# Optimization experiments

Measured on AMD Instinct MI355X. Metric: run time of the kernel, lower is better.

The kernel has to match this reference:

```python
import jax, jax.numpy as jnp
import numpy as np

HEADS = 8
EMBED = 512


def setup_inputs() -> dict:
    key = jax.random.key(0)
    ks = jax.random.split(key, 9)
    N, KL, QL, S = 4, 512, 32, 64
    D = EMBED // HEADS
    return {
        "values": jax.random.normal(ks[0], (N, KL, EMBED), jnp.float32),
        "keys": jax.random.normal(ks[1], (N, KL, EMBED), jnp.float32),
        "query": jax.random.normal(ks[2], (N, QL, S, EMBED), jnp.float32),
        "mask": jax.random.randint(ks[3], (N, 1, 1, KL, 1), 0, 2, jnp.int32),
        "Wv": jax.random.normal(ks[4], (D, D), jnp.float32) * 0.05,
        "Wk": jax.random.normal(ks[5], (D, D), jnp.float32) * 0.05,
        "Wq": jax.random.normal(ks[6], (D, D), jnp.float32) * 0.05,
        "Wo": jax.random.normal(ks[7], (EMBED, EMBED), jnp.float32) * 0.05,
        "bo": jax.random.normal(ks[8], (EMBED,), jnp.float32) * 0.05,
    }


def reference(values, keys, query, mask, Wv, Wk, Wq, Wo, bo):
    N, KL, E = keys.shape
    QL, S = query.shape[1], query.shape[2]
    H = HEADS
    D = E // H
    # split heads, then per-head linear (weights shared across heads, torch y = x @ W.T)
    v = jnp.einsum('nkhd,ed->nkhe', values.reshape(N, KL, H, D), Wv)
    k = jnp.einsum('nkhd,ed->nkhe', keys.reshape(N, KL, H, D), Wk)
    q = jnp.einsum('nqshd,ed->nqshe', query.reshape(N, QL, S, H, D), Wq)
    # energy: [N, H, QL, KL, S]
    energy = jnp.einsum('nqshd,nkhd->nhqks', q, k)
    energy = jnp.where(mask == 0, jnp.float32(-1e20), energy)
    scale = jnp.float32(E ** 0.5)
    attention = jax.nn.softmax(energy / scale, axis=3)  # softmax over key axis
    out = jnp.einsum('nhqks,nkhd->nqshd', attention, v).reshape(N, QL, S, E)
    return out @ Wo.T + bo
```

## Files before the change

kernel.cpp:

```cpp
#include <hip/hip_runtime.h>
#include <math.h>


typedef __bf16 bf16;
typedef __attribute__((ext_vector_type(8))) __bf16 bf16x8;
typedef __attribute__((ext_vector_type(4))) __bf16 bf16x4;
typedef __attribute__((ext_vector_type(4))) float f32x4;

#define LW 68
#define LS 72
#define QSCALE (0.044194173824159216f * 1.4426950408889634f)
#define MASK_BIAS -64.0f

__device__ __forceinline__ bf16x8 cvt8(const float* p, float s) {
    float4 x0 = *(const float4*)p;
    float4 x1 = *(const float4*)(p + 4);
    bf16x8 r = {(bf16)(x0.x * s), (bf16)(x0.y * s), (bf16)(x0.z * s), (bf16)(x0.w * s),
                (bf16)(x1.x * s), (bf16)(x1.y * s), (bf16)(x1.z * s), (bf16)(x1.w * s)};
    return r;
}

__global__ __launch_bounds__(256, 2) void kv_proj(const float* __restrict__ keys,
                                                  const float* __restrict__ values,
                                                  const float* __restrict__ Wk,
                                                  const float* __restrict__ Wv,
                                                  bf16* __restrict__ Kp,
                                                  bf16* __restrict__ Vt) {
    __shared__ bf16 Xk[64 * LW];
    __shared__ bf16 Xv[64 * LW];
    int t = threadIdx.x;
    int nh = blockIdx.x >> 3, kt = blockIdx.x & 7;
    int n = nh >> 3, h = nh & 7, kl0 = kt * 64;
    int w = t >> 6, quad = (t >> 4) & 3, c16 = t & 15;
#pragma unroll
    for (int i = 0; i < 4; ++i) {
        int f = t + i * 256, row = f >> 4, c4 = f & 15;
        float4 a = *(const float4*)(keys + ((long)n * 512 + kl0 + row) * 512 + h * 64 + c4 * 4);
        float4 b = *(const float4*)(values + ((long)n * 512 + kl0 + row) * 512 + h * 64 + c4 * 4);
        *(bf16x4*)&Xk[row * LW + c4 * 4] = (bf16x4){(bf16)a.x, (bf16)a.y, (bf16)a.z, (bf16)a.w};
        *(bf16x4*)&Xv[row * LW + c4 * 4] = (bf16x4){(bf16)b.x, (bf16)b.y, (bf16)b.z, (bf16)b.w};
    }
    __syncthreads();
    if (w < 2) {
        bf16x8 wf[8];
#pragma unroll
        for (int nb = 0; nb < 4; ++nb)
#pragma unroll
            for (int kc = 0; kc < 2; ++kc)
                wf[nb * 2 + kc] = cvt8(Wk + (16 * nb + c16) * 64 + 32 * kc + quad * 8, 1.0f);
        f32x4 acc[2][4];
#pragma unroll
        for (int mb = 0; mb < 2; ++mb)
#pragma unroll
            for (int nb = 0; nb < 4; ++nb) acc[mb][nb] = (f32x4){0.f, 0.f, 0.f, 0.f};
#pragma unroll
        for (int kc = 0; kc < 2; ++kc) {
            bf16x8 a0 = *(const bf16x8*)&Xk[(32 * w + c16) * LW + 32 * kc + quad * 8];
            bf16x8 a1 = *(const bf16x8*)&Xk[(32 * w + 16 + c16) * LW + 32 * kc + quad * 8];
#pragma unroll
            for (int nb = 0; nb < 4; ++nb) {
                acc[0][nb] = __builtin_amdgcn_mfma_f32_16x16x32_bf16(a0, wf[nb * 2 + kc], acc[0][nb], 0, 0, 0);
                acc[1][nb] = __builtin_amdgcn_mfma_f32_16x16x32_bf16(a1, wf[nb * 2 + kc], acc[1][nb], 0, 0, 0);
            }
        }
#pragma unroll
        for (int mb = 0; mb < 2; ++mb)
#pragma unroll
            for (int nb = 0; nb < 4; ++nb)
#pragma unroll
                for (int r = 0; r < 4; ++r)
                    Kp[((long)nh * 512 + kl0 + 32 * w + 16 * mb + quad * 4 + r) * 64 + 16 * nb + c16] =
                        (bf16)acc[mb][nb][r];
    } else {
        int w2 = w - 2;
        bf16x8 af[4];
#pragma unroll
        for (int mb = 0; mb < 2; ++mb)
#pragma unroll
            for (int kc = 0; kc < 2; ++kc)
                af[mb * 2 + kc] = cvt8(Wv + (32 * w2 + 16 * mb + c16) * 64 + 32 * kc + quad * 8, 1.0f);
        f32x4 acc[2][4];
#pragma unroll
        for (int mb = 0; mb < 2; ++mb)
#pragma unroll
            for (int nb = 0; nb < 4; ++nb) acc[mb][nb] = (f32x4){0.f, 0.f, 0.f, 0.f};
#pragma unroll
        for (int kc = 0; kc < 2; ++kc) {
#pragma unroll
            for (int nb = 0; nb < 4; ++nb) {
                bf16x8 b = *(const bf16x8*)&Xv[(16 * nb + c16) * LW + 32 * kc + quad * 8];
                acc[0][nb] = __builtin_amdgcn_mfma_f32_16x16x32_bf16(af[kc], b, acc[0][nb], 0, 0, 0);
                acc[1][nb] = __builtin_amdgcn_mfma_f32_16x16x32_bf16(af[2 + kc], b, acc[1][nb], 0, 0, 0);
            }
        }
#pragma unroll
        for (int mb = 0; mb < 2; ++mb)
#pragma unroll
            for (int nb = 0; nb < 4; ++nb)
#pragma unroll
                for (int r = 0; r < 4; ++r)
                    Vt[((long)nh * 64 + 32 * w2 + 16 * mb + quad * 4 + r) * 512 + kl0 + 16 * nb + c16] =
                        (bf16)acc[mb][nb][r];
    }
}

__global__ __launch_bounds__(256, 3) void attn(const float* __restrict__ query,
                                               const float* __restrict__ Wq,
                                               const bf16* __restrict__ Kp,
                                               const bf16* __restrict__ Vtg,
                                               const int* __restrict__ mask,
                                               bf16* __restrict__ AO) {
    __shared__ bf16 SX[128 * LS];
    __shared__ bf16 Qt[128 * LW];
    __shared__ bf16 Kt[64 * LW];
    __shared__ bf16 Vs[64 * LW];
    __shared__ float Mb[64];
    int t = threadIdx.x;
    int nh = blockIdx.x & 31, qtile = blockIdx.x >> 5;
    int n = nh >> 3, h = nh & 7;
    int r0 = qtile * 128;
    int w = t >> 6, quad = (t >> 4) & 3, c16 = t & 15;
    const bf16* Kb = Kp + (long)nh * 512 * 64;
    const bf16* Vb = Vtg + (long)nh * 64 * 512;

    int prow0 = t >> 3, pcol0 = t & 7;
    int prow1 = (t + 256) >> 3, pcol1 = t & 7;
    bf16x8 pk0 = *(const bf16x8*)(Kb + (long)prow0 * 64 + pcol0 * 8);
    bf16x8 pk1 = *(const bf16x8*)(Kb + (long)prow1 * 64 + pcol1 * 8);
    bf16x8 pv0 = *(const bf16x8*)(Vb + (long)prow0 * 512 + pcol0 * 8);
    bf16x8 pv1 = *(const bf16x8*)(Vb + (long)prow1 * 512 + pcol1 * 8);
    float mnext = 0.f;
    if (t < 64) mnext = mask[n * 512 + t] ? 0.f : MASK_BIAS;

    bf16x8 wf[8];
#pragma unroll
    for (int nb = 0; nb < 4; ++nb)
#pragma unroll
        for (int kc = 0; kc < 2; ++kc)
            wf[nb * 2 + kc] = cvt8(Wq + (16 * nb + c16) * 64 + 32 * kc + quad * 8, QSCALE);

#pragma unroll
    for (int i = 0; i < 8; ++i) {
        int f = t + i * 256, row = f >> 4, c4 = f & 15;
        float4 a = *(const float4*)(query + ((long)n * 2048 + r0 + row) * 512 + h * 64 + c4 * 4);
        *(bf16x4*)&SX[row * LS + c4 * 4] = (bf16x4){(bf16)a.x, (bf16)a.y, (bf16)a.z, (bf16)a.w};
    }
    __syncthreads();
    {
        f32x4 qa[2][4];
#pragma unroll
        for (int mb = 0; mb < 2; ++mb)
#pragma unroll
            for (int nb = 0; nb < 4; ++nb) qa[mb][nb] = (f32x4){0.f, 0.f, 0.f, 0.f};
#pragma unroll
        for (int kc = 0; kc < 2; ++kc) {
            bf16x8 a0 = *(const bf16x8*)&SX[(32 * w + c16) * LS + 32 * kc + quad * 8];
            bf16x8 a1 = *(const bf16x8*)&SX[(32 * w + 16 + c16) * LS + 32 * kc + quad * 8];
#pragma unroll
            for (int nb = 0; nb < 4; ++nb) {
                qa[0][nb] = __builtin_amdgcn_mfma_f32_16x16x32_bf16(a0, wf[nb * 2 + kc], qa[0][nb], 0, 0, 0);
                qa[1][nb] = __builtin_amdgcn_mfma_f32_16x16x32_bf16(a1, wf[nb * 2 + kc], qa[1][nb], 0, 0, 0);
            }
        }
#pragma unroll
        for (int mb = 0; mb < 2; ++mb)
#pragma unroll
            for (int nb = 0; nb < 4; ++nb)
#pragma unroll
                for (int r = 0; r < 4; ++r)
                    Qt[(32 * w + 16 * mb + quad * 4 + r) * LW + 16 * nb + c16] = (bf16)qa[mb][nb][r];
    }

    f32x4 oacc[4][2];
#pragma unroll
    for (int mb = 0; mb < 4; ++mb)
#pragma unroll
        for (int nb = 0; nb < 2; ++nb) oacc[mb][nb] = (f32x4){0.f, 0.f, 0.f, 0.f};
    float ps[2] = {0.f, 0.f};

    for (int kt = 0; kt < 8; ++kt) {
        if (kt) __syncthreads();
        *(bf16x8*)&Kt[prow0 * LW + pcol0 * 8] = pk0;
        *(bf16x8*)&Kt[prow1 * LW + pcol1 * 8] = pk1;
        *(bf16x8*)&Vs[prow0 * LW + pcol0 * 8] = pv0;
        *(bf16x8*)&Vs[prow1 * LW + pcol1 * 8] = pv1;
        if (t < 64) Mb[t] = mnext;
        __syncthreads();
        if (kt < 7) {
            const bf16* Kn = Kb + (long)(kt + 1) * 64 * 64;
            const bf16* Vn = Vb + (kt + 1) * 64;
            pk0 = *(const bf16x8*)(Kn + (long)prow0 * 64 + pcol0 * 8);
            pk1 = *(const bf16x8*)(Kn + (long)prow1 * 64 + pcol1 * 8);
            pv0 = *(const bf16x8*)(Vn + (long)prow0 * 512 + pcol0 * 8);
            pv1 = *(const bf16x8*)(Vn + (long)prow1 * 512 + pcol1 * 8);
            if (t < 64) mnext = mask[n * 512 + (kt + 1) * 64 + t] ? 0.f : MASK_BIAS;
        }
        f32x4 sc[4][2];
#pragma unroll
        for (int mb = 0; mb < 4; ++mb) {
            f32x4 bias = *(const f32x4*)&Mb[16 * mb + quad * 4];
            sc[mb][0] = bias;
            sc[mb][1] = bias;
        }
#pragma unroll
        for (int kc = 0; kc < 2; ++kc) {
            bf16x8 ka[4];
#pragma unroll
            for (int mb = 0; mb < 4; ++mb)
                ka[mb] = *(const bf16x8*)&Kt[(16 * mb + c16) * LW + 32 * kc + quad * 8];
#pragma unroll
            for (int nb = 0; nb < 2; ++nb) {
                bf16x8 qb = *(const bf16x8*)&Qt[(32 * w + 16 * nb + c16) * LW + 32 * kc + quad * 8];
#pragma unroll
                for (int mb = 0; mb < 4; ++mb)
                    sc[mb][nb] = __builtin_amdgcn_mfma_f32_16x16x32_bf16(ka[mb], qb, sc[mb][nb], 0, 0, 0);
            }
        }
#pragma unroll
        for (int mb = 0; mb < 4; ++mb)
#pragma unroll
            for (int nb = 0; nb < 2; ++nb) {
                float p0 = exp2f(sc[mb][nb][0]);
                float p1 = exp2f(sc[mb][nb][1]);
                float p2 = exp2f(sc[mb][nb][2]);
                float p3 = exp2f(sc[mb][nb][3]);
                ps[nb] += (p0 + p1) + (p2 + p3);
                *(bf16x4*)&SX[(32 * w + 16 * nb + c16) * LS + 16 * mb + quad * 4] =
                    (bf16x4){(bf16)p0, (bf16)p1, (bf16)p2, (bf16)p3};
            }
#pragma unroll
        for (int kc = 0; kc < 2; ++kc) {
            bf16x8 va[4];
#pragma unroll
            for (int mb = 0; mb < 4; ++mb)
                va[mb] = *(const bf16x8*)&Vs[(16 * mb + c16) * LW + 32 * kc + quad * 8];
#pragma unroll
            for (int nb = 0; nb < 2; ++nb) {
                bf16x8 pb = *(const bf16x8*)&SX[(32 * w + 16 * nb + c16) * LS + 32 * kc + quad * 8];
#pragma unroll
                for (int mb = 0; mb < 4; ++mb)
                    oacc[mb][nb] = __builtin_amdgcn_mfma_f32_16x16x32_bf16(va[mb], pb, oacc[mb][nb], 0, 0, 0);
            }
        }
    }
#pragma unroll
    for (int nb = 0; nb < 2; ++nb) {
        ps[nb] += __shfl_xor(ps[nb], 16);
        ps[nb] += __shfl_xor(ps[nb], 32);
    }
    float il[2] = {1.0f / ps[0], 1.0f / ps[1]};
#pragma unroll
    for (int mb = 0; mb < 4; ++mb)
#pragma unroll
        for (int nb = 0; nb < 2; ++nb) {
            int row_g = r0 + 32 * w + 16 * nb + c16;
            *(bf16x4*)(AO + ((long)n * 2048 + row_g) * 512 + h * 64 + 16 * mb + quad * 4) =
                (bf16x4){(bf16)(oacc[mb][nb][0] * il[nb]), (bf16)(oacc[mb][nb][1] * il[nb]),
                         (bf16)(oacc[mb][nb][2] * il[nb]), (bf16)(oacc[mb][nb][3] * il[nb])};
        }
}

__global__ __launch_bounds__(256, 2) void out_gemm(const bf16* __restrict__ A,
                                                   const float* __restrict__ Wo,
                                                   const float* __restrict__ bo,
                                                   float* __restrict__ C) {
    __shared__ bf16 At[128 * LW];
    __shared__ bf16 Bt[64 * LW];
    int t = threadIdx.x;
    int br = blockIdx.x & 63, bc = blockIdx.x >> 6;
    int r0 = br * 128, c0 = bc * 64;
    int w = t >> 6, quad = (t >> 4) & 3, c16 = t & 15;
    int arow[4], acol[4];
#pragma unroll
    for (int i = 0; i < 4; ++i) {
        int f = t + i * 256;
        arow[i] = f >> 3;
        acol[i] = f & 7;
    }
    int wrow[4], wcol[4];
#pragma unroll
    for (int i = 0; i < 4; ++i) {
        int f = t + i * 256;
        wrow[i] = f >> 4;
        wcol[i] = f & 15;
    }
    bf16x8 pa[4];
    float4 pw[4];
#pragma unroll
    for (int i = 0; i < 4; ++i) {
        pa[i] = *(const bf16x8*)(A + (long)(r0 + arow[i]) * 512 + acol[i] * 8);
        pw[i] = *(const float4*)(Wo + (long)(c0 + wrow[i]) * 512 + wcol[i] * 4);
    }
    f32x4 acc[2][4];
#pragma unroll
    for (int mb = 0; mb < 2; ++mb)
#pragma unroll
        for (int nb = 0; nb < 4; ++nb) acc[mb][nb] = (f32x4){0.f, 0.f, 0.f, 0.f};
    for (int k0 = 0; k0 < 512; k0 += 64) {
        if (k0) __syncthreads();
#pragma unroll
        for (int i = 0; i < 4; ++i) {
            *(bf16x8*)&At[arow[i] * LW + acol[i] * 8] = pa[i];
            *(bf16x4*)&Bt[wrow[i] * LW + wcol[i] * 4] =
                (bf16x4){(bf16)pw[i].x, (bf16)pw[i].y, (bf16)pw[i].z, (bf16)pw[i].w};
        }
        __syncthreads();
        if (k0 < 448) {
#pragma unroll
            for (int i = 0; i < 4; ++i) {
                pa[i] = *(const bf16x8*)(A + (long)(r0 + arow[i]) * 512 + k0 + 64 + acol[i] * 8);
                pw[i] = *(const float4*)(Wo + (long)(c0 + wrow[i]) * 512 + k0 + 64 + wcol[i] * 4);
            }
        }
#pragma unroll
        for (int kc = 0; kc < 2; ++kc) {
            bf16x8 a0 = *(const bf16x8*)&At[(32 * w + c16) * LW + 32 * kc + quad * 8];
            bf16x8 a1 = *(const bf16x8*)&At[(32 * w + 16 + c16) * LW + 32 * kc + quad * 8];
#pragma unroll
            for (int nb = 0; nb < 4; ++nb) {
                bf16x8 b = *(const bf16x8*)&Bt[(16 * nb + c16) * LW + 32 * kc + quad * 8];
                acc[0][nb] = __builtin_amdgcn_mfma_f32_16x16x32_bf16(a0, b, acc[0][nb], 0, 0, 0);
                acc[1][nb] = __builtin_amdgcn_mfma_f32_16x16x32_bf16(a1, b, acc[1][nb], 0, 0, 0);
            }
        }
    }
#pragma unroll
    for (int mb = 0; mb < 2; ++mb)
#pragma unroll
        for (int nb = 0; nb < 4; ++nb) {
            float bias = bo[c0 + 16 * nb + c16];
#pragma unroll
            for (int r = 0; r < 4; ++r)
                C[(long)(r0 + 32 * w + 16 * mb + quad * 4 + r) * 512 + c0 + 16 * nb + c16] =
                    acc[mb][nb][r] + bias;
        }
}

extern "C" void kernel_launch(void* const* d_in, const int* in_sizes, int n_in,
                              void* d_out, int out_size, void* d_ws, size_t ws_size,
                              hipStream_t stream) {
    const float* values = (const float*)d_in[0];
    const float* keys   = (const float*)d_in[1];
    const float* query  = (const float*)d_in[2];
    const int*   maskp  = (const int*)d_in[3];
    const float* Wv     = (const float*)d_in[4];
    const float* Wk     = (const float*)d_in[5];
    const float* Wq     = (const float*)d_in[6];
    const float* Wo     = (const float*)d_in[7];
    const float* bo     = (const float*)d_in[8];
    float* out = (float*)d_out;

    bf16* ws = (bf16*)d_ws;
    bf16* Kp = ws;
    bf16* Vt = Kp + 1048576;
    bf16* AO = Vt + 1048576;

    kv_proj<<<dim3(256), dim3(256), 0, stream>>>(keys, values, Wk, Wv, Kp, Vt);
    attn<<<dim3(512), dim3(256), 0, stream>>>(query, Wq, Kp, Vt, maskp, AO);
    out_gemm<<<dim3(512), dim3(256), 0, stream>>>(AO, Wo, bo, out);
}
```

Before: 126.0 us.

## Load K/V fragments straight from global memory in attention, dropping LDS staging

The attention kernel no longer stages K, V and mask tiles through shared memory with double-buffered register prefetch and two barriers per key tile. Each wave now loads its K/V MFMA fragments and mask values directly from global memory (relying on L1/L2 reuse), and Q fragments are hoisted into registers once before the loop. This removes the barriers and LDS traffic, but adds redundant global loads across the four waves and exposes load latency without explicit prefetch. Some cosmetic cleanup in cvt8 and out_gemm index setup is included.

```diff
diff --git a/kernel.cpp b/kernel.cpp
--- a/kernel.cpp
+++ b/kernel.cpp
@@ -15,9 +15,8 @@
 __device__ __forceinline__ bf16x8 cvt8(const float* p, float s) {
     float4 x0 = *(const float4*)p;
     float4 x1 = *(const float4*)(p + 4);
-    bf16x8 r = {(bf16)(x0.x * s), (bf16)(x0.y * s), (bf16)(x0.z * s), (bf16)(x0.w * s),
-                (bf16)(x1.x * s), (bf16)(x1.y * s), (bf16)(x1.z * s), (bf16)(x1.w * s)};
-    return r;
+    return (bf16x8){(bf16)(x0.x * s), (bf16)(x0.y * s), (bf16)(x0.z * s), (bf16)(x0.w * s),
+                    (bf16)(x1.x * s), (bf16)(x1.y * s), (bf16)(x1.z * s), (bf16)(x1.w * s)};
 }
 
 __global__ __launch_bounds__(256, 2) void kv_proj(const float* __restrict__ keys,
@@ -108,13 +107,10 @@
                                                const float* __restrict__ Wq,
                                                const bf16* __restrict__ Kp,
                                                const bf16* __restrict__ Vtg,
-                                               const int* __restrict__ mask,
+                                               const int* __restrict__ maskp,
                                                bf16* __restrict__ AO) {
     __shared__ bf16 SX[128 * LS];
     __shared__ bf16 Qt[128 * LW];
-    __shared__ bf16 Kt[64 * LW];
-    __shared__ bf16 Vs[64 * LW];
-    __shared__ float Mb[64];
     int t = threadIdx.x;
     int nh = blockIdx.x & 31, qtile = blockIdx.x >> 5;
     int n = nh >> 3, h = nh & 7;
@@ -123,15 +119,6 @@
     const bf16* Kb = Kp + (long)nh * 512 * 64;
     const bf16* Vb = Vtg + (long)nh * 64 * 512;
 
-    int prow0 = t >> 3, pcol0 = t & 7;
-    int prow1 = (t + 256) >> 3, pcol1 = t & 7;
-    bf16x8 pk0 = *(const bf16x8*)(Kb + (long)prow0 * 64 + pcol0 * 8);
-    bf16x8 pk1 = *(const bf16x8*)(Kb + (long)prow1 * 64 + pcol1 * 8);
-    bf16x8 pv0 = *(const bf16x8*)(Vb + (long)prow0 * 512 + pcol0 * 8);
-    bf16x8 pv1 = *(const bf16x8*)(Vb + (long)prow1 * 512 + pcol1 * 8);
-    float mnext = 0.f;
-    if (t < 64) mnext = mask[n * 512 + t] ? 0.f : MASK_BIAS;
-
     bf16x8 wf[8];
 #pragma unroll
     for (int nb = 0; nb < 4; ++nb)
@@ -170,6 +157,12 @@
                 for (int r = 0; r < 4; ++r)
                     Qt[(32 * w + 16 * mb + quad * 4 + r) * LW + 16 * nb + c16] = (bf16)qa[mb][nb][r];
     }
+    bf16x8 qf[2][2];
+#pragma unroll
+    for (int nb = 0; nb < 2; ++nb)
+#pragma unroll
+        for (int kc = 0; kc < 2; ++kc)
+            qf[nb][kc] = *(const bf16x8*)&Qt[(32 * w + 16 * nb + c16) * LW + 32 * kc + quad * 8];
 
     f32x4 oacc[4][2];
 #pragma unroll
@@ -179,26 +172,15 @@
     float ps[2] = {0.f, 0.f};
 
     for (int kt = 0; kt < 8; ++kt) {
-        if (kt) __syncthreads();
-        *(bf16x8*)&Kt[prow0 * LW + pcol0 * 8] = pk0;
-        *(bf16x8*)&Kt[prow1 * LW + pcol1 * 8] = pk1;
-        *(bf16x8*)&Vs[prow0 * LW + pcol0 * 8] = pv0;
-        *(bf16x8*)&Vs[prow1 * LW + pcol1 * 8] = pv1;
-        if (t < 64) Mb[t] = mnext;
-        __syncthreads();
-        if (kt < 7) {
-            const bf16* Kn = Kb + (long)(kt + 1) * 64 * 64;
-            const bf16* Vn = Vb + (kt + 1) * 64;
-            pk0 = *(const bf16x8*)(Kn + (long)prow0 * 64 + pcol0 * 8);
-            pk1 = *(const bf16x8*)(Kn + (long)prow1 * 64 + pcol1 * 8);
-            pv0 = *(const bf16x8*)(Vn + (long)prow0 * 512 + pcol0 * 8);
-            pv1 = *(const bf16x8*)(Vn + (long)prow1 * 512 + pcol1 * 8);
-            if (t < 64) mnext = mask[n * 512 + (kt + 1) * 64 + t] ? 0.f : MASK_BIAS;
-        }
+        int4 mk[4];
+#pragma unroll
+        for (int mb = 0; mb < 4; ++mb)
+            mk[mb] = *(const int4*)(maskp + n * 512 + kt * 64 + 16 * mb + quad * 4);
         f32x4 sc[4][2];
 #pragma unroll
         for (int mb = 0; mb < 4; ++mb) {
-            f32x4 bias = *(const f32x4*)&Mb[16 * mb + quad * 4];
+            f32x4 bias = {mk[mb].x ? 0.f : MASK_BIAS, mk[mb].y ? 0.f : MASK_BIAS,
+                          mk[mb].z ? 0.f : MASK_BIAS, mk[mb].w ? 0.f : MASK_BIAS};
             sc[mb][0] = bias;
             sc[mb][1] = bias;
         }
@@ -207,14 +189,12 @@
             bf16x8 ka[4];
 #pragma unroll
             for (int mb = 0; mb < 4; ++mb)
-                ka[mb] = *(const bf16x8*)&Kt[(16 * mb + c16) * LW + 32 * kc + quad * 8];
-#pragma unroll
-            for (int nb = 0; nb < 2; ++nb) {
-                bf16x8 qb = *(const bf16x8*)&Qt[(32 * w + 16 * nb + c16) * LW + 32 * kc + quad * 8];
+                ka[mb] = *(const bf16x8*)(Kb + (long)(kt * 64 + 16 * mb + c16) * 64 + 32 * kc + quad * 8);
+#pragma unroll
+            for (int nb = 0; nb < 2; ++nb)
 #pragma unroll
                 for (int mb = 0; mb < 4; ++mb)
-                    sc[mb][nb] = __builtin_amdgcn_mfma_f32_16x16x32_bf16(ka[mb], qb, sc[mb][nb], 0, 0, 0);
-            }
+                    sc[mb][nb] = __builtin_amdgcn_mfma_f32_16x16x32_bf16(ka[mb], qf[nb][kc], sc[mb][nb], 0, 0, 0);
         }
 #pragma unroll
         for (int mb = 0; mb < 4; ++mb)
@@ -233,7 +213,7 @@
             bf16x8 va[4];
 #pragma unroll
             for (int mb = 0; mb < 4; ++mb)
-                va[mb] = *(const bf16x8*)&Vs[(16 * mb + c16) * LW + 32 * kc + quad * 8];
+                va[mb] = *(const bf16x8*)(Vb + (long)(16 * mb + c16) * 512 + kt * 64 + 32 * kc + quad * 8);
 #pragma unroll
             for (int nb = 0; nb < 2; ++nb) {
                 bf16x8 pb = *(const bf16x8*)&SX[(32 * w + 16 * nb + c16) * LS + 32 * kc + quad * 8];
@@ -270,17 +250,12 @@
     int br = blockIdx.x & 63, bc = blockIdx.x >> 6;
     int r0 = br * 128, c0 = bc * 64;
     int w = t >> 6, quad = (t >> 4) & 3, c16 = t & 15;
-    int arow[4], acol[4];
+    int arow[4], acol[4], wrow[4], wcol[4];
 #pragma unroll
     for (int i = 0; i < 4; ++i) {
         int f = t + i * 256;
         arow[i] = f >> 3;
         acol[i] = f & 7;
-    }
-    int wrow[4], wcol[4];
-#pragma unroll
-    for (int i = 0; i < 4; ++i) {
-        int f = t + i * 256;
         wrow[i] = f >> 4;
         wcol[i] = f & 15;
     }
```

Result: slower. 137.9 us (+9.5%).

## Halve attention query tile to 64 rows, double grid, drop Qt buffer

Applied to the files above, without the earlier changes.

The attention kernel now processes 64 query rows per block instead of 128, so each wave owns 16 rows, and the grid doubles to 1024 blocks. Each wave loads and projects only its own query rows, which removes the block-wide sync before the Q projection. The projected Q tile is written back into SX and kept in registers, so the separate Qt shared buffer is gone. Launch bounds rise to 4 blocks per CU, trading more K/V tile reloads per query row for lower shared memory and register use, higher occupancy and more blocks to spread across CUs.

```diff
diff --git a/kernel.cpp b/kernel.cpp
--- a/kernel.cpp
+++ b/kernel.cpp
@@ -15,9 +15,8 @@
 __device__ __forceinline__ bf16x8 cvt8(const float* p, float s) {
     float4 x0 = *(const float4*)p;
     float4 x1 = *(const float4*)(p + 4);
-    bf16x8 r = {(bf16)(x0.x * s), (bf16)(x0.y * s), (bf16)(x0.z * s), (bf16)(x0.w * s),
-                (bf16)(x1.x * s), (bf16)(x1.y * s), (bf16)(x1.z * s), (bf16)(x1.w * s)};
-    return r;
+    return (bf16x8){(bf16)(x0.x * s), (bf16)(x0.y * s), (bf16)(x0.z * s), (bf16)(x0.w * s),
+                    (bf16)(x1.x * s), (bf16)(x1.y * s), (bf16)(x1.z * s), (bf16)(x1.w * s)};
 }
 
 __global__ __launch_bounds__(256, 2) void kv_proj(const float* __restrict__ keys,
@@ -104,21 +103,20 @@
     }
 }
 
-__global__ __launch_bounds__(256, 3) void attn(const float* __restrict__ query,
+__global__ __launch_bounds__(256, 4) void attn(const float* __restrict__ query,
                                                const float* __restrict__ Wq,
                                                const bf16* __restrict__ Kp,
                                                const bf16* __restrict__ Vtg,
-                                               const int* __restrict__ mask,
+                                               const int* __restrict__ maskp,
                                                bf16* __restrict__ AO) {
-    __shared__ bf16 SX[128 * LS];
-    __shared__ bf16 Qt[128 * LW];
+    __shared__ bf16 SX[64 * LS];
     __shared__ bf16 Kt[64 * LW];
     __shared__ bf16 Vs[64 * LW];
     __shared__ float Mb[64];
     int t = threadIdx.x;
     int nh = blockIdx.x & 31, qtile = blockIdx.x >> 5;
     int n = nh >> 3, h = nh & 7;
-    int r0 = qtile * 128;
+    int r0 = qtile * 64;
     int w = t >> 6, quad = (t >> 4) & 3, c16 = t & 15;
     const bf16* Kb = Kp + (long)nh * 512 * 64;
     const bf16* Vb = Vtg + (long)nh * 64 * 512;
@@ -130,7 +128,7 @@
     bf16x8 pv0 = *(const bf16x8*)(Vb + (long)prow0 * 512 + pcol0 * 8);
     bf16x8 pv1 = *(const bf16x8*)(Vb + (long)prow1 * 512 + pcol1 * 8);
     float mnext = 0.f;
-    if (t < 64) mnext = mask[n * 512 + t] ? 0.f : MASK_BIAS;
+    if (t < 64) mnext = maskp[n * 512 + t] ? 0.f : MASK_BIAS;
 
     bf16x8 wf[8];
 #pragma unroll
@@ -139,44 +137,41 @@
         for (int kc = 0; kc < 2; ++kc)
             wf[nb * 2 + kc] = cvt8(Wq + (16 * nb + c16) * 64 + 32 * kc + quad * 8, QSCALE);
 
-#pragma unroll
-    for (int i = 0; i < 8; ++i) {
-        int f = t + i * 256, row = f >> 4, c4 = f & 15;
-        float4 a = *(const float4*)(query + ((long)n * 2048 + r0 + row) * 512 + h * 64 + c4 * 4);
-        *(bf16x4*)&SX[row * LS + c4 * 4] = (bf16x4){(bf16)a.x, (bf16)a.y, (bf16)a.z, (bf16)a.w};
-    }
-    __syncthreads();
     {
-        f32x4 qa[2][4];
-#pragma unroll
-        for (int mb = 0; mb < 2; ++mb)
-#pragma unroll
-            for (int nb = 0; nb < 4; ++nb) qa[mb][nb] = (f32x4){0.f, 0.f, 0.f, 0.f};
-#pragma unroll
-        for (int kc = 0; kc < 2; ++kc) {
-            bf16x8 a0 = *(const bf16x8*)&SX[(32 * w + c16) * LS + 32 * kc + quad * 8];
-            bf16x8 a1 = *(const bf16x8*)&SX[(32 * w + 16 + c16) * LS + 32 * kc + quad * 8];
-#pragma unroll
-            for (int nb = 0; nb < 4; ++nb) {
-                qa[0][nb] = __builtin_amdgcn_mfma_f32_16x16x32_bf16(a0, wf[nb * 2 + kc], qa[0][nb], 0, 0, 0);
-                qa[1][nb] = __builtin_amdgcn_mfma_f32_16x16x32_bf16(a1, wf[nb * 2 + kc], qa[1][nb], 0, 0, 0);
-            }
-        }
-#pragma unroll
-        for (int mb = 0; mb < 2; ++mb)
-#pragma unroll
-            for (int nb = 0; nb < 4; ++nb)
-#pragma unroll
-                for (int r = 0; r < 4; ++r)
-                    Qt[(32 * w + 16 * mb + quad * 4 + r) * LW + 16 * nb + c16] = (bf16)qa[mb][nb][r];
-    }
-
-    f32x4 oacc[4][2];
-#pragma unroll
-    for (int mb = 0; mb < 4; ++mb)
-#pragma unroll
-        for (int nb = 0; nb < 2; ++nb) oacc[mb][nb] = (f32x4){0.f, 0.f, 0.f, 0.f};
-    float ps[2] = {0.f, 0.f};
+        int l = t & 63;
+        int rloc = 16 * w + (l >> 2);
+        const float* qrow = query + ((long)n * 2048 + r0 + rloc) * 512 + h * 64;
+#pragma unroll
+        for (int j = 0; j < 4; ++j) {
+            int c = (l & 3) + 4 * j;
+            float4 a = *(const float4*)(qrow + c * 4);
+            *(bf16x4*)&SX[rloc * LS + c * 4] = (bf16x4){(bf16)a.x, (bf16)a.y, (bf16)a.z, (bf16)a.w};
+        }
+    }
+    f32x4 qa[4];
+#pragma unroll
+    for (int nb = 0; nb < 4; ++nb) qa[nb] = (f32x4){0.f, 0.f, 0.f, 0.f};
+#pragma unroll
+    for (int kc = 0; kc < 2; ++kc) {
+        bf16x8 a = *(const bf16x8*)&SX[(16 * w + c16) * LS + 32 * kc + quad * 8];
+#pragma unroll
+        for (int nb = 0; nb < 4; ++nb)
+            qa[nb] = __builtin_amdgcn_mfma_f32_16x16x32_bf16(a, wf[nb * 2 + kc], qa[nb], 0, 0, 0);
+    }
+#pragma unroll
+    for (int nb = 0; nb < 4; ++nb)
+#pragma unroll
+        for (int r = 0; r < 4; ++r)
+            SX[(16 * w + quad * 4 + r) * LS + 16 * nb + c16] = (bf16)qa[nb][r];
+    bf16x8 qf[2];
+#pragma unroll
+    for (int kc = 0; kc < 2; ++kc)
+        qf[kc] = *(const bf16x8*)&SX[(16 * w + c16) * LS + 32 * kc + quad * 8];
+
+    f32x4 oacc[4];
+#pragma unroll
+    for (int mb = 0; mb < 4; ++mb) oacc[mb] = (f32x4){0.f, 0.f, 0.f, 0.f};
+    float ps = 0.f;
 
     for (int kt = 0; kt < 8; ++kt) {
         if (kt) __syncthreads();
@@ -193,71 +188,48 @@
             pk1 = *(const bf16x8*)(Kn + (long)prow1 * 64 + pcol1 * 8);
             pv0 = *(const bf16x8*)(Vn + (long)prow0 * 512 + pcol0 * 8);
             pv1 = *(const bf16x8*)(Vn + (long)prow1 * 512 + pcol1 * 8);
-            if (t < 64) mnext = mask[n * 512 + (kt + 1) * 64 + t] ? 0.f : MASK_BIAS;
-        }
-        f32x4 sc[4][2];
+            if (t < 64) mnext = maskp[n * 512 + (kt + 1) * 64 + t] ? 0.f : MASK_BIAS;
+        }
+        f32x4 sc[4];
+#pragma unroll
+        for (int mb = 0; mb < 4; ++mb) sc[mb] = *(const f32x4*)&Mb[16 * mb + quad * 4];
+#pragma unroll
+        for (int kc = 0; kc < 2; ++kc) {
+#pragma unroll
+            for (int mb = 0; mb < 4; ++mb) {
+                bf16x8 ka = *(const bf16x8*)&Kt[(16 * mb + c16) * LW + 32 * kc + quad * 8];
+                sc[mb] = __builtin_amdgcn_mfma_f32_16x16x32_bf16(ka, qf[kc], sc[mb], 0, 0, 0);
+            }
+        }
 #pragma unroll
         for (int mb = 0; mb < 4; ++mb) {
-            f32x4 bias = *(const f32x4*)&Mb[16 * mb + quad * 4];
-            sc[mb][0] = bias;
-            sc[mb][1] = bias;
-        }
-#pragma unroll
-        for (int kc = 0; kc < 2; ++kc) {
-            bf16x8 ka[4];
-#pragma unroll
-            for (int mb = 0; mb < 4; ++mb)
-                ka[mb] = *(const bf16x8*)&Kt[(16 * mb + c16) * LW + 32 * kc + quad * 8];
-#pragma unroll
-            for (int nb = 0; nb < 2; ++nb) {
-                bf16x8 qb = *(const bf16x8*)&Qt[(32 * w + 16 * nb + c16) * LW + 32 * kc + quad * 8];
-#pragma unroll
-                for (int mb = 0; mb < 4; ++mb)
-                    sc[mb][nb] = __builtin_amdgcn_mfma_f32_16x16x32_bf16(ka[mb], qb, sc[mb][nb], 0, 0, 0);
-            }
-        }
-#pragma unroll
-        for (int mb = 0; mb < 4; ++mb)
-#pragma unroll
-            for (int nb = 0; nb < 2; ++nb) {
-                float p0 = exp2f(sc[mb][nb][0]);
-                float p1 = exp2f(sc[mb][nb][1]);
-                float p2 = exp2f(sc[mb][nb][2]);
-                float p3 = exp2f(sc[mb][nb][3]);
-                ps[nb] += (p0 + p1) + (p2 + p3);
-                *(bf16x4*)&SX[(32 * w + 16 * nb + c16) * LS + 16 * mb + quad * 4] =
-                    (bf16x4){(bf16)p0, (bf16)p1, (bf16)p2, (bf16)p3};
-            }
-#pragma unroll
-        for (int kc = 0; kc < 2; ++kc) {
-            bf16x8 va[4];
-#pragma unroll
-            for (int mb = 0; mb < 4; ++mb)
-                va[mb] = *(const bf16x8*)&Vs[(16 * mb + c16) * LW + 32 * kc + quad * 8];
-#pragma unroll
-            for (int nb = 0; nb < 2; ++nb) {
-                bf16x8 pb = *(const bf16x8*)&SX[(32 * w + 16 * nb + c16) * LS + 32 * kc + quad * 8];
-#pragma unroll
-                for (int mb = 0; mb < 4; ++mb)
-                    oacc[mb][nb] = __builtin_amdgcn_mfma_f32_16x16x32_bf16(va[mb], pb, oacc[mb][nb], 0, 0, 0);
-            }
-        }
-    }
-#pragma unroll
-    for (int nb = 0; nb < 2; ++nb) {
-        ps[nb] += __shfl_xor(ps[nb], 16);
-        ps[nb] += __shfl_xor(ps[nb], 32);
-    }
-    float il[2] = {1.0f / ps[0], 1.0f / ps[1]};
+            float p0 = exp2f(sc[mb][0]);
+            float p1 = exp2f(sc[mb][1]);
+            float p2 = exp2f(sc[mb][2]);
+            float p3 = exp2f(sc[mb][3]);
+            ps += (p0 + p1) + (p2 + p3);
+            *(bf16x4*)&SX[(16 * w + c16) * LS + 16 * mb + quad * 4] =
+                (bf16x4){(bf16)p0, (bf16)p1, (bf16)p2, (bf16)p3};
+        }
+#pragma unroll
+        for (int kc = 0; kc < 2; ++kc) {
+            bf16x8 pb = *(const bf16x8*)&SX[(16 * w + c16) * LS + 32 * kc + quad * 8];
+#pragma unroll
+            for (int mb = 0; mb < 4; ++mb) {
+                bf16x8 va = *(const bf16x8*)&Vs[(16 * mb + c16) * LW + 32 * kc + quad * 8];
+                oacc[mb] = __builtin_amdgcn_mfma_f32_16x16x32_bf16(va, pb, oacc[mb], 0, 0, 0);
+            }
+        }
+    }
+    ps += __shfl_xor(ps, 16);
+    ps += __shfl_xor(ps, 32);
+    float il = 1.0f / ps;
+    int row_g = r0 + 16 * w + c16;
 #pragma unroll
     for (int mb = 0; mb < 4; ++mb)
-#pragma unroll
-        for (int nb = 0; nb < 2; ++nb) {
-            int row_g = r0 + 32 * w + 16 * nb + c16;
-            *(bf16x4*)(AO + ((long)n * 2048 + row_g) * 512 + h * 64 + 16 * mb + quad * 4) =
-                (bf16x4){(bf16)(oacc[mb][nb][0] * il[nb]), (bf16)(oacc[mb][nb][1] * il[nb]),
-                         (bf16)(oacc[mb][nb][2] * il[nb]), (bf16)(oacc[mb][nb][3] * il[nb])};
-        }
+        *(bf16x4*)(AO + ((long)n * 2048 + row_g) * 512 + h * 64 + 16 * mb + quad * 4) =
+            (bf16x4){(bf16)(oacc[mb][0] * il), (bf16)(oacc[mb][1] * il),
+                     (bf16)(oacc[mb][2] * il), (bf16)(oacc[mb][3] * il)};
 }
 
 __global__ __launch_bounds__(256, 2) void out_gemm(const bf16* __restrict__ A,
@@ -270,17 +242,12 @@
     int br = blockIdx.x & 63, bc = blockIdx.x >> 6;
     int r0 = br * 128, c0 = bc * 64;
     int w = t >> 6, quad = (t >> 4) & 3, c16 = t & 15;
-    int arow[4], acol[4];
+    int arow[4], acol[4], wrow[4], wcol[4];
 #pragma unroll
     for (int i = 0; i < 4; ++i) {
         int f = t + i * 256;
         arow[i] = f >> 3;
         acol[i] = f & 7;
-    }
-    int wrow[4], wcol[4];
-#pragma unroll
-    for (int i = 0; i < 4; ++i) {
-        int f = t + i * 256;
         wrow[i] = f >> 4;
         wcol[i] = f & 15;
     }
@@ -356,6 +323,6 @@
     bf16* AO = Vt + 1048576;
 
     kv_proj<<<dim3(256), dim3(256), 0, stream>>>(keys, values, Wk, Wv, Kp, Vt);
-    attn<<<dim3(512), dim3(256), 0, stream>>>(query, Wq, Kp, Vt, maskp, AO);
+    attn<<<dim3(1024), dim3(256), 0, stream>>>(query, Wq, Kp, Vt, maskp, AO);
     out_gemm<<<dim3(512), dim3(256), 0, stream>>>(AO, Wo, bo, out);
 }
```

Measured after the change: 129.0 us. 2.4% more time.
